# Kernel tuning notes

Measured on AMD Instinct MI355X. Metric: run time of the kernel, lower is better.

## Reference

```python
import jax, jax.numpy as jnp
import numpy as np

N, C, H, K = 32768, 128, 4, 16
D = C // H  # head_dim = 32


def setup_inputs() -> dict:
    key = jax.random.key(0)
    ks = jax.random.split(key, 8)
    feats = jax.random.normal(ks[0], (N, C), dtype=jnp.float32)
    coords = jax.random.normal(ks[1], (N, 3), dtype=jnp.float32)
    knn_idx = jax.random.randint(ks[2], (N, K), 0, N, dtype=jnp.int64)
    s = 0.02
    Wq = jax.random.normal(ks[3], (C, C), dtype=jnp.float32) * s
    Wk = jax.random.normal(ks[4], (C, C), dtype=jnp.float32) * s
    Wv = jax.random.normal(ks[5], (C, C), dtype=jnp.float32) * s
    Wo = jax.random.normal(ks[6], (C, C), dtype=jnp.float32) * s
    bo = jnp.zeros((C,), dtype=jnp.float32)
    return {"feats": feats, "coords": coords, "knn_idx": knn_idx,
            "Wq": Wq, "Wk": Wk, "Wv": Wv, "Wo": Wo, "bo": bo}


def reference(feats, coords, knn_idx, Wq, Wk, Wv, Wo, bo):
    # coords only feeds the kNN search (precomputed as knn_idx)
    n, c = feats.shape
    q = (feats @ Wq.T).reshape(n, H, D)          # [N,H,D]
    k = (feats @ Wk.T).reshape(n, H, D)          # [N,H,D]
    v = (feats @ Wv.T).reshape(n, H, D)          # [N,H,D]
    kn = k[knn_idx]                               # gather -> [N,K,H,D]
    vn = v[knn_idx]                               # gather -> [N,K,H,D]
    scores = jnp.einsum('nhd,nkhd->nhk', q, kn) / jnp.sqrt(jnp.float32(D))
    w = jax.nn.softmax(scores, axis=-1)           # softmax over K neighbors
    out = jnp.einsum('nhk,nkhd->nhd', w, vn).reshape(n, c)
    return out @ Wo.T + bo
```

## Files before the change

### kernel.cpp

```cpp
#include <hip/hip_runtime.h>

#define NPTS 32768
#define C 128
#define KNBR 16

typedef __attribute__((ext_vector_type(8))) short short8;
typedef __attribute__((ext_vector_type(4))) float floatx4;
typedef __attribute__((ext_vector_type(4))) int intx4;

#define QSCALE 1.4f
__device__ __forceinline__ ushort f2b(float f) {
    union { float f; uint u; } x; x.f = f;
    uint r = (x.u + 0x7fffu + ((x.u >> 16) & 1u)) >> 16;
    return (ushort)r;
}

__global__ __launch_bounds__(256) void prep_all(
    const float* __restrict__ feats, const float* __restrict__ Wq,
    const float* __restrict__ Wk, const float* __restrict__ Wv,
    const float* __restrict__ Wo,
    ushort* __restrict__ feats_b, ushort* __restrict__ wfq,
    ushort* __restrict__ wfk, ushort* __restrict__ wfv, ushort* __restrict__ wfo)
{
    const int b = blockIdx.x, tid = threadIdx.x;
    if (b < 2048) {
        const size_t i = (size_t)b * 2048 + (size_t)tid * 8;
        float4 v0 = *(const float4*)(feats + i);
        float4 v1 = *(const float4*)(feats + i + 4);
        intx4 o;
        o.x = (int)((uint)f2b(v0.x) | ((uint)f2b(v0.y) << 16));
        o.y = (int)((uint)f2b(v0.z) | ((uint)f2b(v0.w) << 16));
        o.z = (int)((uint)f2b(v1.x) | ((uint)f2b(v1.y) << 16));
        o.w = (int)((uint)f2b(v1.z) | ((uint)f2b(v1.w) << 16));
        *(intx4*)(feats_b + i) = o;
        return;
    }
    const int wb = b - 2048;
    const int wsel = wb >> 3;
    const int tg = (wb & 7) * 256 + tid;
    const int colblk = tg >> 8;
    const int rem = tg & 255;
    const int kk = rem >> 6, kb = (rem >> 4) & 3, fr = rem & 15;
    const int col = colblk * 16 + fr;
    const int kbase = (kk * 4 + kb) * 8;

    const float* src = (wsel == 0) ? Wq : (wsel == 1) ? Wk : (wsel == 2) ? Wv : Wo;
    ushort* dst = (wsel == 0) ? wfq : (wsel == 1) ? wfk : (wsel == 2) ? wfv : wfo;

    ushort tmp[8];
#pragma unroll
    for (int e = 0; e < 8; ++e) tmp[e] = f2b(src[(size_t)col * 128 + kbase + e]);
    intx4 o;
    o.x = (int)((uint)tmp[0] | ((uint)tmp[1] << 16));
    o.y = (int)((uint)tmp[2] | ((uint)tmp[3] << 16));
    o.z = (int)((uint)tmp[4] | ((uint)tmp[5] << 16));
    o.w = (int)((uint)tmp[6] | ((uint)tmp[7] << 16));
    *(intx4*)(dst + (size_t)tg * 8) = o;
}

__global__ __launch_bounds__(256) void qkv_gemm(
    const ushort* __restrict__ A,
    const ushort* __restrict__ wfq, const ushort* __restrict__ wfk,
    const ushort* __restrict__ wfv,
    unsigned char* __restrict__ q8, unsigned char* __restrict__ kv8)
{
    __shared__ ushort ldsA[32 * 128];
    const int tid = threadIdx.x, lane = tid & 63, wid = tid >> 6;
    const int r0 = blockIdx.x * 32, sel = blockIdx.y;
    const ushort* WF = (sel == 0) ? wfq : (sel == 1) ? wfk : wfv;

#pragma unroll
    for (int it = 0; it < 2; ++it) {
        const int f = it * 256 + tid;
        const int row = f >> 4, slot = f & 15;
        intx4 v = *(const intx4*)(A + (size_t)r0 * 128 + (size_t)f * 8);
        *(intx4*)(ldsA + ((row * 16 + (slot ^ (row & 7))) * 8)) = v;
    }
    __syncthreads();

    const int fr = lane & 15, kb = lane >> 4;

    short8 af[2][4];
#pragma unroll
    for (int i = 0; i < 2; ++i)
#pragma unroll
        for (int kk = 0; kk < 4; ++kk) {
            const int row = i * 16 + fr;
            const int slot = kk * 4 + kb;
            af[i][kk] = *(const short8*)(ldsA + ((row * 16 + (slot ^ (row & 7))) * 8));
        }

    floatx4 acc[2][2];
#pragma unroll
    for (int i = 0; i < 2; ++i)
#pragma unroll
        for (int j = 0; j < 2; ++j) acc[i][j] = (floatx4){0.f, 0.f, 0.f, 0.f};

#pragma unroll
    for (int kk = 0; kk < 4; ++kk) {
        short8 bf[2];
#pragma unroll
        for (int j = 0; j < 2; ++j)
            bf[j] = *(const short8*)(WF + ((size_t)(wid * 2 + j) * 256 + kk * 64 + lane) * 8);
#pragma unroll
        for (int i = 0; i < 2; ++i)
#pragma unroll
            for (int j = 0; j < 2; ++j)
                acc[i][j] = __builtin_amdgcn_mfma_f32_16x16x32_bf16(af[i][kk], bf[j], acc[i][j], 0, 0, 0);
    }

    const float qs = 127.f / QSCALE;
    const int boff = (wid * 8 + (fr >> 1)) * 4;
#pragma unroll
    for (int i = 0; i < 2; ++i)
#pragma unroll
        for (int r = 0; r < 4; ++r) {
            const int nn = r0 + i * 16 + kb * 4 + r;
            float f0 = fminf(fmaxf(acc[i][0][r] * qs, -127.f), 127.f);
            float f1 = fminf(fmaxf(acc[i][1][r] * qs, -127.f), 127.f);
            int b0 = __float2int_rn(f0);
            int b1 = __float2int_rn(f1);
            uint u16 = (uint)(b0 & 0xff) | ((uint)(b1 & 0xff) << 8);
            uint o16 = __shfl_xor(u16, 1);
            if (!(fr & 1)) {
                const uint word = u16 | (o16 << 16);
                if (sel == 0)      *(uint*)(q8  + (size_t)nn * 128 + boff) = word;
                else if (sel == 1) *(uint*)(kv8 + (size_t)nn * 256 + boff) = word;
                else               *(uint*)(kv8 + (size_t)nn * 256 + 128 + boff) = word;
            }
        }
}

__global__ __launch_bounds__(256, 6) void attn_kernel(
    const unsigned char* __restrict__ q8, const unsigned char* __restrict__ kv8,
    const int* __restrict__ knn, ushort* __restrict__ attn_p)
{
    const int tid = threadIdx.x;
    const int lane = tid & 63;
    const int wp = __builtin_amdgcn_readfirstlane(tid >> 6);
    const int n = blockIdx.x * 4 + wp;

    const int kk = lane >> 2, h = lane & 3;
    const int nb4 = knn[(size_t)n * KNBR + kk];
    const int* kr = knn + (size_t)n * KNBR;

    const unsigned char* krow = kv8 + (size_t)nb4 * 256 + h * 32;
    intx4 k0 = *(const intx4*)(krow);
    intx4 k1 = *(const intx4*)(krow + 16);
    const unsigned char* qrow = q8 + (size_t)n * 128 + h * 32;
    intx4 qq0 = *(const intx4*)(qrow);
    intx4 qq1 = *(const intx4*)(qrow + 16);

    ushort vsh[KNBR];
#pragma unroll
    for (int j = 0; j < KNBR; ++j) {
        const int nbv = kr[j];
        vsh[j] = *(const ushort*)(kv8 + (size_t)nbv * 256 + 128 + lane * 2);
    }

    int dp = 0;
#if __has_builtin(__builtin_amdgcn_sdot4)
#pragma unroll
    for (int i = 0; i < 4; ++i) dp = __builtin_amdgcn_sdot4(qq0[i], k0[i], dp, false);
#pragma unroll
    for (int i = 0; i < 4; ++i) dp = __builtin_amdgcn_sdot4(qq1[i], k1[i], dp, false);
#else
#pragma unroll
    for (int i = 0; i < 4; ++i) {
        uint a = (uint)qq0[i], b = (uint)k0[i];
        dp += (int)(signed char)(a) * (int)(signed char)(b)
            + (int)(signed char)(a >> 8) * (int)(signed char)(b >> 8)
            + (int)(signed char)(a >> 16) * (int)(signed char)(b >> 16)
            + (int)(signed char)(a >> 24) * (int)(signed char)(b >> 24);
        a = (uint)qq1[i]; b = (uint)k1[i];
        dp += (int)(signed char)(a) * (int)(signed char)(b)
            + (int)(signed char)(a >> 8) * (int)(signed char)(b >> 8)
            + (int)(signed char)(a >> 16) * (int)(signed char)(b >> 16)
            + (int)(signed char)(a >> 24) * (int)(signed char)(b >> 24);
    }
#endif

    const float SCORE_F = (QSCALE / 127.f) * (QSCALE / 127.f) * 0.17677669529663687f;
    const float sc = (float)dp * SCORE_F;

    float mxv = sc;
    mxv = fmaxf(mxv, __shfl_xor(mxv, 4));
    mxv = fmaxf(mxv, __shfl_xor(mxv, 8));
    mxv = fmaxf(mxv, __shfl_xor(mxv, 16));
    mxv = fmaxf(mxv, __shfl_xor(mxv, 32));
    const float e = __expf(sc - mxv);
    float sm = e;
    sm += __shfl_xor(sm, 4);
    sm += __shfl_xor(sm, 8);
    sm += __shfl_xor(sm, 16);
    sm += __shfl_xor(sm, 32);
    const float wgt = e * (QSCALE / 127.f) / sm;

    const int h2v = lane >> 4;
    float a0 = 0.f, a1 = 0.f;
#pragma unroll
    for (int j = 0; j < KNBR; ++j) {
        const float w2 = __shfl(wgt, j * 4 + h2v);
        const ushort u = vsh[j];
        a0 += w2 * (float)(signed char)(u & 0xff);
        a1 += w2 * (float)(signed char)(u >> 8);
    }
    const int cb = 32 * (lane >> 4) + (lane & 15);
    attn_p[(size_t)n * 128 + cb]      = f2b(a0);
    attn_p[(size_t)n * 128 + cb + 16] = f2b(a1);
}

__global__ __launch_bounds__(256) void out_gemm(
    const ushort* __restrict__ A, const ushort* __restrict__ wfo,
    const float* __restrict__ bias, float* __restrict__ out)
{
    __shared__ ushort ldsA[32 * 128];
    const int tid = threadIdx.x, lane = tid & 63, wid = tid >> 6;
    const int r0 = blockIdx.x * 32;

#pragma unroll
    for (int it = 0; it < 2; ++it) {
        const int f = it * 256 + tid;
        const int row = f >> 4, slot = f & 15;
        intx4 v = *(const intx4*)(A + (size_t)r0 * 128 + (size_t)f * 8);
        *(intx4*)(ldsA + ((row * 16 + (slot ^ (row & 7))) * 8)) = v;
    }
    __syncthreads();

    const int fr = lane & 15, kb = lane >> 4;

    short8 af[2][4];
#pragma unroll
    for (int i = 0; i < 2; ++i)
#pragma unroll
        for (int kk = 0; kk < 4; ++kk) {
            const int row = i * 16 + fr;
            const int slot = kk * 4 + kb;
            af[i][kk] = *(const short8*)(ldsA + ((row * 16 + (slot ^ (row & 7))) * 8));
        }

    floatx4 acc[2][2];
#pragma unroll
    for (int i = 0; i < 2; ++i)
#pragma unroll
        for (int j = 0; j < 2; ++j) acc[i][j] = (floatx4){0.f, 0.f, 0.f, 0.f};

#pragma unroll
    for (int kk = 0; kk < 4; ++kk) {
        short8 bf[2];
#pragma unroll
        for (int j = 0; j < 2; ++j)
            bf[j] = *(const short8*)(wfo + ((size_t)(wid * 2 + j) * 256 + kk * 64 + lane) * 8);
#pragma unroll
        for (int i = 0; i < 2; ++i)
#pragma unroll
            for (int j = 0; j < 2; ++j)
                acc[i][j] = __builtin_amdgcn_mfma_f32_16x16x32_bf16(af[i][kk], bf[j], acc[i][j], 0, 0, 0);
    }

#pragma unroll
    for (int j = 0; j < 2; ++j) {
        const int col = wid * 32 + j * 16 + fr;
        const float bv = bias[col];
#pragma unroll
        for (int i = 0; i < 2; ++i)
#pragma unroll
            for (int r = 0; r < 4; ++r) {
                const int n = r0 + i * 16 + kb * 4 + r;
                out[(size_t)n * 128 + col] = acc[i][j][r] + bv;
            }
    }
}

extern "C" void kernel_launch(void* const* d_in, const int* in_sizes, int n_in,
                              void* d_out, int out_size, void* d_ws, size_t ws_size,
                              hipStream_t stream)
{
    const float* feats = (const float*)d_in[0];
    const int*   knn   = (const int*)d_in[2];
    const float* Wq    = (const float*)d_in[3];
    const float* Wk    = (const float*)d_in[4];
    const float* Wv    = (const float*)d_in[5];
    const float* Wo    = (const float*)d_in[6];
    const float* bo    = (const float*)d_in[7];
    float* out = (float*)d_out;

    ushort* feats_b = (ushort*)d_ws;
    ushort* attn_p  = feats_b + (size_t)NPTS * C;
    unsigned char* q8  = (unsigned char*)(attn_p + (size_t)NPTS * C);
    unsigned char* kv8 = q8 + (size_t)NPTS * 128;
    ushort* wfq    = (ushort*)(kv8 + (size_t)NPTS * 256);
    ushort* wfk    = wfq + 16384;
    ushort* wfv    = wfk + 16384;
    ushort* wfo    = wfv + 16384;

    prep_all<<<2080, 256, 0, stream>>>(feats, Wq, Wk, Wv, Wo,
                                       feats_b, wfq, wfk, wfv, wfo);
    qkv_gemm<<<dim3(NPTS / 32, 3), 256, 0, stream>>>(feats_b, wfq, wfk, wfv, q8, kv8);
    attn_kernel<<<NPTS / 4, 256, 0, stream>>>(q8, kv8, knn, attn_p);
    out_gemm<<<NPTS / 32, 256, 0, stream>>>(attn_p, wfo, bo, out);
}
```

Measured before the change: 42.85 us.

## Fuse feats bf16 conversion into QKV GEMM load and raise attn occupancy

Drops the separate pass that converted feats to bf16 in workspace. The QKV GEMM now reads fp32 feats directly and converts while staging into LDS, and the prep kernel only handles the weights. This removes a full write-then-read of an 8 MB bf16 copy, but each of the three sel blocks now reads fp32 feats (twice the bytes) and converts it redundantly. Attention kernel launch bounds also change from 6 to 8 waves per SIMD, which may force register spilling.

```diff
diff --git a/kernel.cpp b/kernel.cpp
--- a/kernel.cpp
+++ b/kernel.cpp
@@ -15,29 +15,15 @@
     return (ushort)r;
 }
 
-__global__ __launch_bounds__(256) void prep_all(
-    const float* __restrict__ feats, const float* __restrict__ Wq,
-    const float* __restrict__ Wk, const float* __restrict__ Wv,
-    const float* __restrict__ Wo,
-    ushort* __restrict__ feats_b, ushort* __restrict__ wfq,
-    ushort* __restrict__ wfk, ushort* __restrict__ wfv, ushort* __restrict__ wfo)
+__global__ __launch_bounds__(256) void prep_w(
+    const float* __restrict__ Wq, const float* __restrict__ Wk,
+    const float* __restrict__ Wv, const float* __restrict__ Wo,
+    ushort* __restrict__ wfq, ushort* __restrict__ wfk,
+    ushort* __restrict__ wfv, ushort* __restrict__ wfo)
 {
     const int b = blockIdx.x, tid = threadIdx.x;
-    if (b < 2048) {
-        const size_t i = (size_t)b * 2048 + (size_t)tid * 8;
-        float4 v0 = *(const float4*)(feats + i);
-        float4 v1 = *(const float4*)(feats + i + 4);
-        intx4 o;
-        o.x = (int)((uint)f2b(v0.x) | ((uint)f2b(v0.y) << 16));
-        o.y = (int)((uint)f2b(v0.z) | ((uint)f2b(v0.w) << 16));
-        o.z = (int)((uint)f2b(v1.x) | ((uint)f2b(v1.y) << 16));
-        o.w = (int)((uint)f2b(v1.z) | ((uint)f2b(v1.w) << 16));
-        *(intx4*)(feats_b + i) = o;
-        return;
-    }
-    const int wb = b - 2048;
-    const int wsel = wb >> 3;
-    const int tg = (wb & 7) * 256 + tid;
+    const int wsel = b >> 3;
+    const int tg = (b & 7) * 256 + tid;
     const int colblk = tg >> 8;
     const int rem = tg & 255;
     const int kk = rem >> 6, kb = (rem >> 4) & 3, fr = rem & 15;
@@ -59,7 +45,7 @@
 }
 
 __global__ __launch_bounds__(256) void qkv_gemm(
-    const ushort* __restrict__ A,
+    const float* __restrict__ feats,
     const ushort* __restrict__ wfq, const ushort* __restrict__ wfk,
     const ushort* __restrict__ wfv,
     unsigned char* __restrict__ q8, unsigned char* __restrict__ kv8)
@@ -69,12 +55,20 @@
     const int r0 = blockIdx.x * 32, sel = blockIdx.y;
     const ushort* WF = (sel == 0) ? wfq : (sel == 1) ? wfk : wfv;
 
-#pragma unroll
-    for (int it = 0; it < 2; ++it) {
+    float4 va[4];
+#pragma unroll
+    for (int it = 0; it < 4; ++it) {
         const int f = it * 256 + tid;
-        const int row = f >> 4, slot = f & 15;
-        intx4 v = *(const intx4*)(A + (size_t)r0 * 128 + (size_t)f * 8);
-        *(intx4*)(ldsA + ((row * 16 + (slot ^ (row & 7))) * 8)) = v;
+        va[it] = *(const float4*)(feats + (size_t)r0 * 128 + (size_t)f * 4);
+    }
+#pragma unroll
+    for (int it = 0; it < 4; ++it) {
+        const int f = it * 256 + tid;
+        const int row = f >> 5, slot = (f & 31) >> 1, half = f & 1;
+        uint2 o;
+        o.x = (uint)f2b(va[it].x) | ((uint)f2b(va[it].y) << 16);
+        o.y = (uint)f2b(va[it].z) | ((uint)f2b(va[it].w) << 16);
+        *(uint2*)(ldsA + (row * 16 + (slot ^ (row & 7))) * 8 + half * 4) = o;
     }
     __syncthreads();
 
@@ -131,7 +125,7 @@
         }
 }
 
-__global__ __launch_bounds__(256, 6) void attn_kernel(
+__global__ __launch_bounds__(256, 8) void attn_kernel(
     const unsigned char* __restrict__ q8, const unsigned char* __restrict__ kv8,
     const int* __restrict__ knn, ushort* __restrict__ attn_p)
 {
@@ -285,8 +279,7 @@
     const float* bo    = (const float*)d_in[7];
     float* out = (float*)d_out;
 
-    ushort* feats_b = (ushort*)d_ws;
-    ushort* attn_p  = feats_b + (size_t)NPTS * C;
+    ushort* attn_p = (ushort*)d_ws;
     unsigned char* q8  = (unsigned char*)(attn_p + (size_t)NPTS * C);
     unsigned char* kv8 = q8 + (size_t)NPTS * 128;
     ushort* wfq    = (ushort*)(kv8 + (size_t)NPTS * 256);
@@ -294,9 +287,8 @@
     ushort* wfv    = wfk + 16384;
     ushort* wfo    = wfv + 16384;
 
-    prep_all<<<2080, 256, 0, stream>>>(feats, Wq, Wk, Wv, Wo,
-                                       feats_b, wfq, wfk, wfv, wfo);
-    qkv_gemm<<<dim3(NPTS / 32, 3), 256, 0, stream>>>(feats_b, wfq, wfk, wfv, q8, kv8);
+    prep_w<<<32, 256, 0, stream>>>(Wq, Wk, Wv, Wo, wfq, wfk, wfv, wfo);
+    qkv_gemm<<<dim3(NPTS / 32, 3), 256, 0, stream>>>(feats, wfq, wfk, wfv, q8, kv8);
     attn_kernel<<<NPTS / 4, 256, 0, stream>>>(q8, kv8, knn, attn_p);
     out_gemm<<<NPTS / 32, 256, 0, stream>>>(attn_p, wfo, bo, out);
 }
```

Measured after the change: 45.01 us. +5.0%, slower.
